# Optimization experiments

Hardware: AMD Instinct MI355X
Metric: run time of the kernel (lower is better)

The kernel has to match this reference:

```python
import jax, jax.numpy as jnp
import numpy as np

N_QUBITS = 4
N_LAYERS = 2


def _apply_1q(state, gate, wire):
    # state: [B,2,2,2,2] complex; gate: [2,2] or [B,2,2] complex
    ax = wire + 1
    st = jnp.moveaxis(state, ax, 1)  # [B,2,...]
    if gate.ndim == 2:
        st = jnp.einsum('ij,bj...->bi...', gate, st)
    else:
        st = jnp.einsum('bij,bj...->bi...', gate, st)
    return jnp.moveaxis(st, 1, ax)


def _cnot(state, control, target):
    ca, ta = control + 1, target + 1
    s0 = jnp.take(state, 0, axis=ca)
    s1 = jnp.take(state, 1, axis=ca)
    ta2 = ta - 1 if ta > ca else ta  # axis shift after take
    s1 = jnp.flip(s1, axis=ta2)      # flip target when control=1
    return jnp.stack([s0, s1], axis=ca)


def _rx(theta):  # theta: [B] -> [B,2,2]
    c = jnp.cos(theta / 2).astype(jnp.complex64)
    s = jnp.sin(theta / 2).astype(jnp.complex64)
    return jnp.stack([jnp.stack([c, -1j * s], -1),
                      jnp.stack([-1j * s, c], -1)], -2)


def _ry(theta):  # scalar -> [2,2]
    c = jnp.cos(theta / 2).astype(jnp.complex64)
    s = jnp.sin(theta / 2).astype(jnp.complex64)
    return jnp.stack([jnp.stack([c, -s]), jnp.stack([s, c])])


def _rz(theta):  # scalar -> [2,2] diag(e^{-i t/2}, e^{i t/2})
    half = (theta / 2).astype(jnp.complex64)
    z = jnp.zeros((), jnp.complex64)
    return jnp.stack([jnp.stack([jnp.exp(-1j * half), z]),
                      jnp.stack([z, jnp.exp(1j * half)])])


def _circuit(angles, wq):
    # angles: [B,4] float32; wq: [2,4,3] float32 -> [B,4] expval PauliZ
    B = angles.shape[0]
    state = jnp.zeros((B, 2, 2, 2, 2), jnp.complex64)
    state = state.at[:, 0, 0, 0, 0].set(1.0)
    for i in range(N_QUBITS):
        state = _apply_1q(state, _rx(angles[:, i]), i)
    for layer in range(N_LAYERS):
        for i in range(N_QUBITS):
            state = _apply_1q(state, _rz(wq[layer, i, 0]), i)
            state = _apply_1q(state, _ry(wq[layer, i, 1]), i)
            state = _apply_1q(state, _rz(wq[layer, i, 2]), i)
        for i in range(N_QUBITS - 1):
            state = _cnot(state, i, i + 1)
    probs = state.real ** 2 + state.imag ** 2  # [B,2,2,2,2]
    zs = []
    for i in range(N_QUBITS):
        axes = tuple(a for a in range(1, 5) if a != i + 1)
        marg = jnp.sum(probs, axis=axes)  # [B,2]
        zs.append(marg[:, 0] - marg[:, 1])
    return jnp.stack(zs, axis=-1)  # [B,4]


def setup_inputs() -> dict:
    key = jax.random.key(0)
    ks = jax.random.split(key, 8)
    B, F = 262144, 64
    x = jax.random.normal(ks[0], (B, F), jnp.float32)
    Wp = jax.random.normal(ks[1], (N_QUBITS, F), jnp.float32) * (1.0 / np.sqrt(F))
    bp = jnp.zeros((N_QUBITS,), jnp.float32)
    wq = 0.01 * jax.random.normal(ks[2], (N_LAYERS, N_QUBITS, 3), jnp.float32)
    W1 = jax.random.normal(ks[3], (64, N_QUBITS), jnp.float32) * 0.5
    b1 = jnp.zeros((64,), jnp.float32)
    W2 = jax.random.normal(ks[4], (1, 64), jnp.float32) * 0.125
    b2 = jnp.zeros((1,), jnp.float32)
    return {"x": x, "Wp": Wp, "bp": bp, "wq": wq, "W1": W1, "b1": b1, "W2": W2, "b2": b2}


def reference(x, Wp, bp, wq, W1, b1, W2, b2):
    angles = x @ Wp.T + bp               # feature_projector -> [B,4]
    q_out = _circuit(angles, wq)         # [B,4]
    h = jax.nn.relu(q_out @ W1.T + b1)   # [B,64]
    return h @ W2.T + b2                 # [B,1]
```

## Files before the change

kernel.cpp:

```cpp
#include <hip/hip_runtime.h>
#include <hip/hip_bf16.h>

#define CBUF_N 1157


__device__ inline void gate_rz(float* ar, float* ai, int q, float th) {
    float c = cosf(0.5f * th), s = sinf(0.5f * th);
    int st = 8 >> q;
    #pragma unroll
    for (int k = 0; k < 16; k++) {
        float r = ar[k], im = ai[k];
        if (k & st) {
            ar[k] = r * c - im * s;
            ai[k] = im * c + r * s;
        } else {
            ar[k] = r * c + im * s;
            ai[k] = im * c - r * s;
        }
    }
}

__device__ inline void gate_ry(float* ar, float* ai, int q, float th) {
    float c = cosf(0.5f * th), s = sinf(0.5f * th);
    int st = 8 >> q;
    #pragma unroll
    for (int k = 0; k < 16; k++) {
        if (!(k & st)) {
            int k1 = k | st;
            float r0 = ar[k], i0 = ai[k], r1 = ar[k1], i1 = ai[k1];
            ar[k]  = c * r0 - s * r1;  ai[k]  = c * i0 - s * i1;
            ar[k1] = s * r0 + c * r1;  ai[k1] = s * i0 + c * i1;
        }
    }
}

__device__ inline void gate_cnot(float* ar, float* ai, int c, int t) {
    int stc = 8 >> c, stt = 8 >> t;
    #pragma unroll
    for (int k = 0; k < 16; k++) {
        if ((k & stc) && !(k & stt)) {
            int k1 = k | stt;
            float r = ar[k], im = ai[k];
            ar[k] = ar[k1]; ai[k] = ai[k1];
            ar[k1] = r;     ai[k1] = im;
        }
    }
}

__global__ void precompute_kernel(const float* __restrict__ Wp,
                                  const float* __restrict__ bp,
                                  const float* __restrict__ wq,
                                  const float* __restrict__ W1,
                                  const float* __restrict__ b1,
                                  const float* __restrict__ W2,
                                  const float* __restrict__ b2,
                                  float* __restrict__ ws) {
    int t = threadIdx.x;

    if (t < 16) {
        float ar[16], ai[16];
        #pragma unroll
        for (int k = 0; k < 16; k++) { ar[k] = 0.f; ai[k] = 0.f; }
        ar[t] = 1.f;

        for (int layer = 0; layer < 2; layer++) {
            for (int q = 0; q < 4; q++) {
                const float* w = &wq[(layer * 4 + q) * 3];
                gate_rz(ar, ai, q, w[0]);
                gate_ry(ar, ai, q, w[1]);
                gate_rz(ar, ai, q, w[2]);
            }
            for (int c = 0; c < 3; c++) gate_cnot(ar, ai, c, c + 1);
        }

        int pc = __popc(t) & 3;
        #pragma unroll
        for (int j = 0; j < 16; j++) {
            float re = ar[j], im = ai[j], vr, vi;
            switch (pc) {
                case 0: vr = re;  vi = im;  break;
                case 1: vr = im;  vi = -re; break;
                case 2: vr = -re; vi = -im; break;
                case 3: vr = -im; vi = re;  break;
            }
            ws[j * 16 + t]       = vr;
            ws[256 + j * 16 + t] = vi;
        }
    }

    for (int q = 0; q < 4; q++) ws[512 + t * 4 + q] = Wp[q * 64 + t];
    if (t < 4) ws[768 + t] = bp[t];

    ws[772 + t * 6 + 0] = W1[t * 4 + 0];
    ws[772 + t * 6 + 1] = W1[t * 4 + 1];
    ws[772 + t * 6 + 2] = W1[t * 4 + 2];
    ws[772 + t * 6 + 3] = W1[t * 4 + 3];
    ws[772 + t * 6 + 4] = b1[t];
    ws[772 + t * 6 + 5] = W2[t];
    if (t == 0) ws[1156] = b2[0];
}


__global__ __launch_bounds__(256) void qmain_kernel(const float* __restrict__ x,
                                                    const float* __restrict__ cb,
                                                    float* __restrict__ out,
                                                    int B) {
    int idx = blockIdx.x * 256 + threadIdx.x;
    if (idx >= B) return;

    const float4* x4 = reinterpret_cast<const float4*>(x) + idx * 16;
    float ang[4];
    #pragma unroll
    for (int q = 0; q < 4; q++) ang[q] = cb[768 + q];
    #pragma unroll
    for (int i = 0; i < 16; i++) {
        float4 v = x4[i];
        const float* w = &cb[512 + i * 16];
        #pragma unroll
        for (int q = 0; q < 4; q++) {
            ang[q] += v.x * w[q] + v.y * w[4 + q] + v.z * w[8 + q] + v.w * w[12 + q];
        }
    }

    float c[4], s[4];
    #pragma unroll
    for (int q = 0; q < 4; q++) {
        __sincosf(0.5f * ang[q], &s[q], &c[q]);
    }
    float pre[4]  = { c[0] * c[1], c[0] * s[1], s[0] * c[1], s[0] * s[1] };
    float post[4] = { c[2] * c[3], c[2] * s[3], s[2] * c[3], s[2] * s[3] };
    float m[16];
    #pragma unroll
    for (int k = 0; k < 16; k++) m[k] = pre[k >> 2] * post[k & 3];

    float z0 = 0.f, z1 = 0.f, z2 = 0.f, z3 = 0.f;
    #pragma unroll
    for (int j = 0; j < 16; j++) {
        const float* vr = &cb[j * 16];
        const float* vi = &cb[256 + j * 16];
        float re = 0.f, im = 0.f;
        #pragma unroll
        for (int k = 0; k < 16; k++) {
            re += vr[k] * m[k];
            im += vi[k] * m[k];
        }
        float p = re * re + im * im;
        z0 += (j & 8) ? -p : p;
        z1 += (j & 4) ? -p : p;
        z2 += (j & 2) ? -p : p;
        z3 += (j & 1) ? -p : p;
    }

    float acc = cb[1156];
    #pragma unroll
    for (int j = 0; j < 64; j++) {
        const float* mp = &cb[772 + j * 6];
        float h = mp[4] + mp[0] * z0 + mp[1] * z1 + mp[2] * z2 + mp[3] * z3;
        h = fmaxf(h, 0.f);
        acc += mp[5] * h;
    }
    out[idx] = acc;
}


extern "C" void kernel_launch(void* const* d_in, const int* in_sizes, int n_in,
                              void* d_out, int out_size, void* d_ws, size_t ws_size,
                              hipStream_t stream) {
    const float* x  = (const float*)d_in[0];
    const float* Wp = (const float*)d_in[1];
    const float* bp = (const float*)d_in[2];
    const float* wq = (const float*)d_in[3];
    const float* W1 = (const float*)d_in[4];
    const float* b1 = (const float*)d_in[5];
    const float* W2 = (const float*)d_in[6];
    const float* b2 = (const float*)d_in[7];
    float* ws = (float*)d_ws;
    float* out = (float*)d_out;

    int B = in_sizes[0] / 64;

    precompute_kernel<<<1, 64, 0, stream>>>(Wp, bp, wq, W1, b1, W2, b2, ws);

    int grid = (B + 255) / 256;
    qmain_kernel<<<grid, 256, 0, stream>>>(x, ws, out, B);
}
```

Before: 133.1 us.

## Stage x rows through padded shared memory for coalesced loads

Instead of each thread reading its own 256-byte row with strided float4 loads, the block cooperatively loads 256 rows in two 32-column halves into a padded shared-memory tile, so global reads are coalesced. Each thread then reads its row from LDS for the projection. Several accumulations are also rewritten as explicit fmaf chains. The bounds check on B is removed, so the kernel assumes B is a multiple of 256, and the extra barriers and LDS use may lower occupancy.

After: 124.6 us. 6.4% less time.

```diff
diff --git a/kernel.cpp b/kernel.cpp
--- a/kernel.cpp
+++ b/kernel.cpp
@@ -105,30 +105,45 @@
                                                     const float* __restrict__ cb,
                                                     float* __restrict__ out,
                                                     int B) {
-    int idx = blockIdx.x * 256 + threadIdx.x;
-    if (idx >= B) return;
-
-    const float4* x4 = reinterpret_cast<const float4*>(x) + idx * 16;
+    __shared__ float tile[256 * 33];
+    const int t = threadIdx.x;
+    const long row0 = (long)blockIdx.x * 256;
+    const float* xb = x + row0 * 64;
+
     float ang[4];
     #pragma unroll
     for (int q = 0; q < 4; q++) ang[q] = cb[768 + q];
-    #pragma unroll
-    for (int i = 0; i < 16; i++) {
-        float4 v = x4[i];
-        const float* w = &cb[512 + i * 16];
-        #pragma unroll
-        for (int q = 0; q < 4; q++) {
-            ang[q] += v.x * w[q] + v.y * w[4 + q] + v.z * w[8 + q] + v.w * w[12 + q];
-        }
-    }
-
-    float c[4], s[4];
+
+    #pragma unroll
+    for (int s = 0; s < 2; s++) {
+        if (s) __syncthreads();
+        #pragma unroll
+        for (int r = 0; r < 8; r++) {
+            int idx = r * 1024 + t * 4;
+            int row = idx >> 5;
+            int col = idx & 31;
+            float4 v = *reinterpret_cast<const float4*>(xb + row * 64 + s * 32 + col);
+            float* dst = &tile[row * 33 + col];
+            dst[0] = v.x; dst[1] = v.y; dst[2] = v.z; dst[3] = v.w;
+        }
+        __syncthreads();
+        const float* myrow = &tile[t * 33];
+        #pragma unroll
+        for (int i = 0; i < 32; i++) {
+            float xv = myrow[i];
+            const float* w = &cb[512 + (s * 32 + i) * 4];
+            #pragma unroll
+            for (int q = 0; q < 4; q++) ang[q] = fmaf(xv, w[q], ang[q]);
+        }
+    }
+
+    float c[4], s4[4];
     #pragma unroll
     for (int q = 0; q < 4; q++) {
-        __sincosf(0.5f * ang[q], &s[q], &c[q]);
-    }
-    float pre[4]  = { c[0] * c[1], c[0] * s[1], s[0] * c[1], s[0] * s[1] };
-    float post[4] = { c[2] * c[3], c[2] * s[3], s[2] * c[3], s[2] * s[3] };
+        __sincosf(0.5f * ang[q], &s4[q], &c[q]);
+    }
+    float pre[4]  = { c[0] * c[1], c[0] * s4[1], s4[0] * c[1], s4[0] * s4[1] };
+    float post[4] = { c[2] * c[3], c[2] * s4[3], s4[2] * c[3], s4[2] * s4[3] };
     float m[16];
     #pragma unroll
     for (int k = 0; k < 16; k++) m[k] = pre[k >> 2] * post[k & 3];
@@ -141,8 +156,8 @@
         float re = 0.f, im = 0.f;
         #pragma unroll
         for (int k = 0; k < 16; k++) {
-            re += vr[k] * m[k];
-            im += vi[k] * m[k];
+            re = fmaf(vr[k], m[k], re);
+            im = fmaf(vi[k], m[k], im);
         }
         float p = re * re + im * im;
         z0 += (j & 8) ? -p : p;
@@ -155,11 +170,15 @@
     #pragma unroll
     for (int j = 0; j < 64; j++) {
         const float* mp = &cb[772 + j * 6];
-        float h = mp[4] + mp[0] * z0 + mp[1] * z1 + mp[2] * z2 + mp[3] * z3;
+        float h = mp[4];
+        h = fmaf(mp[0], z0, h);
+        h = fmaf(mp[1], z1, h);
+        h = fmaf(mp[2], z2, h);
+        h = fmaf(mp[3], z3, h);
         h = fmaxf(h, 0.f);
-        acc += mp[5] * h;
-    }
-    out[idx] = acc;
+        acc = fmaf(mp[5], h, acc);
+    }
+    out[row0 + t] = acc;
 }
 
 
```
